# Kernel tuning notes

Hardware: AMD Instinct MI355X
Metric: run time of the kernel (lower is better)

Reference implementation:

```python
import jax, jax.numpy as jnp
import numpy as np

N = 500          # max_neurons, all alive
INPUT_SIZE = 3072
FEAT_DIM = 64
OUT_SIZE = 10
BATCH = 8192
RADIUS = 20.0
VOL = 100.0      # cubic volume (100,100,100)
N_ITER = 3


def setup_inputs() -> dict:
    key = jax.random.key(0)
    k_x, k_pos, k_iw, k_f, k_ow = jax.random.split(key, 5)
    x = jax.random.normal(k_x, (BATCH, INPUT_SIZE), dtype=jnp.float32)
    # seed positions spread across the volume, roughly matching _init_seeds
    positions = jax.random.uniform(k_pos, (N, 3), dtype=jnp.float32) * 80.0 + 10.0
    input_weights = jax.random.normal(k_iw, (N, INPUT_SIZE), dtype=jnp.float32) * 0.02
    features = jax.random.normal(k_f, (N, FEAT_DIM), dtype=jnp.float32) * 0.1
    output_weights = jax.random.normal(k_ow, (N, OUT_SIZE), dtype=jnp.float32) * 0.02
    biases = jnp.zeros((N,), dtype=jnp.float32)
    return {"x": x, "positions": positions, "input_weights": input_weights,
            "features": features, "output_weights": output_weights, "biases": biases}


def reference(x, positions, input_weights, features, output_weights, biases):
    # clamp positions into the volume (per-axis, vol is cubic here)
    pos = jnp.clip(positions, 0.1, VOL - 0.1)  # [N,3]

    # pairwise distances (grad-safe sqrt at the zero diagonal)
    diff = pos[:, None, :] - pos[None, :, :]          # [N,N,3]
    sq = jnp.sum(diff * diff, axis=-1)                # [N,N]
    pos_mask = sq > 0.0
    dist = jnp.where(pos_mask, jnp.sqrt(jnp.where(pos_mask, sq, 1.0)), 0.0)

    conn_mask = (dist < RADIUS) & (dist > 0.0)
    attenuation = jnp.exp(-dist / RADIUS) * conn_mask.astype(dist.dtype)

    # feature similarity (F.normalize clamps the norm from below at eps)
    feat_norm = features / jnp.maximum(
        jnp.linalg.norm(features, axis=1, keepdims=True), 1e-6)
    feat_sim = jnp.clip(feat_norm @ feat_norm.T, -1.0, 1.0)  # [N,N]

    conn_w = attenuation * (0.5 + 0.5 * feat_sim)
    conn_w = conn_w / (jnp.sum(conn_w, axis=1, keepdims=True) + 1e-6)

    # input gating: neurons near x=0 receive input
    x_norm = pos[:, 0] / VOL                          # [N]
    input_weight = jnp.exp(-2.0 * x_norm)
    input_weight = input_weight / (jnp.sum(input_weight) + 1e-6)

    activations = x @ input_weights.T * input_weight + biases  # [B,N]

    # iterative message passing (fixed small iteration count)
    for _ in range(N_ITER):
        msg = activations @ conn_w.T                  # [B,N]
        activations = jnp.minimum(jax.nn.relu(activations + 0.5 * msg), 50.0)

    # output gating: neurons near x=VOL emit output
    output_weight = jnp.exp(2.0 * (x_norm - 1.0))
    output_weight = output_weight / (jnp.sum(output_weight) + 1e-6)

    return activations @ (output_weights * output_weight[:, None])  # [B,OUT]
```

## Files before the change

kernel.cpp:

```cpp
#include <hip/hip_runtime.h>
#include <stdint.h>

#define N_REAL 500
#define NPAD   512
#define K_IN   3072
#define NBATCH 8192
#define NOUT   10
#define RADIUS 20.0f
#define VOLF   100.0f

typedef __attribute__((ext_vector_type(8))) __bf16 bf16x8;
typedef __attribute__((ext_vector_type(4))) float  f32x4;
typedef __attribute__((ext_vector_type(4))) unsigned short us4;

__device__ __forceinline__ unsigned short f2bf(float f) {
    unsigned int u = __float_as_uint(f);
    u += 0x7FFFu + ((u >> 16) & 1u);
    return (unsigned short)(u >> 16);
}
__device__ __forceinline__ float bf2f(unsigned short h) {
    return __uint_as_float(((unsigned int)h) << 16);
}
__device__ __forceinline__ uint2 cvt_pk4(float4 v) {
    uint2 r;
    asm("v_cvt_pk_bf16_f32 %0, %1, %2" : "=v"(r.x) : "v"(v.x), "v"(v.y));
    asm("v_cvt_pk_bf16_f32 %0, %1, %2" : "=v"(r.y) : "v"(v.z), "v"(v.w));
    return r;
}

#define GLOBAL_AS __attribute__((address_space(1)))
#define LDS_AS    __attribute__((address_space(3)))
__device__ __forceinline__ void glds16(const void* g, void* l) {
    __builtin_amdgcn_global_load_lds((const GLOBAL_AS void*)g, (LDS_AS void*)l, 16, 0, 0);
}

__global__ void prep1(const float* __restrict__ positions,
                      const float* __restrict__ features,
                      const float* __restrict__ out_w,
                      const float* __restrict__ biases,
                      float* __restrict__ feat_norm,
                      float* __restrict__ pos_c,
                      float* __restrict__ inw,
                      float* __restrict__ biasp,
                      float* __restrict__ wout)
{
    int n = threadIdx.x;
    float e_in = 0.f, e_out = 0.f;
    float px = 0.f, py = 0.f, pz = 0.f;
    if (n < N_REAL) {
        px = fminf(fmaxf(positions[n*3+0], 0.1f), VOLF - 0.1f);
        py = fminf(fmaxf(positions[n*3+1], 0.1f), VOLF - 0.1f);
        pz = fminf(fmaxf(positions[n*3+2], 0.1f), VOLF - 0.1f);
        float xn = px / VOLF;
        e_in  = expf(-2.f * xn);
        e_out = expf(2.f * (xn - 1.f));
        float ss = 0.f;
        for (int f = 0; f < 64; ++f) { float v = features[n*64+f]; ss += v*v; }
        float nm = fmaxf(sqrtf(ss), 1e-6f);
        for (int f = 0; f < 64; ++f) feat_norm[n*64+f] = features[n*64+f] / nm;
    } else {
        for (int f = 0; f < 64; ++f) feat_norm[n*64+f] = 0.f;
    }
    pos_c[n*4+0] = px; pos_c[n*4+1] = py; pos_c[n*4+2] = pz; pos_c[n*4+3] = 0.f;

    __shared__ float s_in[512], s_out[512];
    s_in[n] = e_in; s_out[n] = e_out;
    __syncthreads();
    for (int s = 256; s > 0; s >>= 1) {
        if (n < s) { s_in[n] += s_in[n+s]; s_out[n] += s_out[n+s]; }
        __syncthreads();
    }
    float sum_in  = s_in[0]  + 1e-6f;
    float sum_out = s_out[0] + 1e-6f;

    inw[n]   = (n < N_REAL) ? (e_in / sum_in) : 0.f;
    biasp[n] = (n < N_REAL) ? biases[n] : 0.f;
    float wo = (n < N_REAL) ? (e_out / sum_out) : 0.f;
    for (int o = 0; o < NOUT; ++o)
        wout[n*NOUT + o] = (n < N_REAL) ? out_w[n*NOUT + o] * wo : 0.f;
}

__global__ void prep2(const float* __restrict__ pos_c,
                      const float* __restrict__ feat_norm,
                      unsigned short* __restrict__ conn_w)
{
    int i = blockIdx.x;
    int t = threadIdx.x;
    __shared__ float fi[64];
    __shared__ float spos[4];
    __shared__ float red[128];
    if (t < 64) fi[t] = feat_norm[i*64 + t];
    if (t < 4)  spos[t] = pos_c[i*4 + t];
    __syncthreads();

    float w[4];
    float part = 0.f;
    for (int jj = 0; jj < 4; ++jj) {
        int j = t + jj*128;
        float val = 0.f;
        if (i < N_REAL && j < N_REAL) {
            float dx = spos[0] - pos_c[j*4+0];
            float dy = spos[1] - pos_c[j*4+1];
            float dz = spos[2] - pos_c[j*4+2];
            float sq = dx*dx + dy*dy + dz*dz;
            if (sq > 0.f) {
                float dist = sqrtf(sq);
                if (dist < RADIUS) {
                    float att = expf(-dist / RADIUS);
                    float sim = 0.f;
                    const float4* fj = (const float4*)(feat_norm + j*64);
                    const float4* fi4 = (const float4*)fi;
                    #pragma unroll
                    for (int f = 0; f < 16; ++f) {
                        float4 a = fi4[f]; float4 b = fj[f];
                        sim += a.x*b.x + a.y*b.y + a.z*b.z + a.w*b.w;
                    }
                    sim = fminf(fmaxf(sim, -1.f), 1.f);
                    val = att * (0.5f + 0.5f*sim);
                }
            }
        }
        w[jj] = val; part += val;
    }
    red[t] = part;
    __syncthreads();
    for (int s = 64; s > 0; s >>= 1) {
        if (t < s) red[t] += red[t+s];
        __syncthreads();
    }
    float inv = 1.f / (red[0] + 1e-6f);
    for (int jj = 0; jj < 4; ++jj)
        conn_w[(long)i*NPAD + t + jj*128] = f2bf(w[jj] * inv);
}

__global__ void cast_pad(const float* __restrict__ src, unsigned short* __restrict__ dst,
                         long total_q, long src_q)
{
    long i = (long)blockIdx.x * blockDim.x + threadIdx.x;
    long stride = (long)gridDim.x * blockDim.x;
    for (; i < total_q; i += stride) {
        us4 o;
        if (i < src_q) {
            float4 v = ((const float4*)src)[i];
            o[0] = f2bf(v.x); o[1] = f2bf(v.y); o[2] = f2bf(v.z); o[3] = f2bf(v.w);
        } else {
            o[0] = 0; o[1] = 0; o[2] = 0; o[3] = 0;
        }
        ((us4*)dst)[i] = o;
    }
}

__device__ __forceinline__ void block_map(int b, int& m0, int& n0) {
    int xcd = b & 7, loc = b >> 3;
    m0 = (xcd*16 + (loc >> 3)) * 64;
    n0 = (loc & 7) * 64;
}

__global__ __launch_bounds__(256)
void gemm1(const float* __restrict__ X,
           const unsigned short* __restrict__ B,
           unsigned short* __restrict__ Cbf,
           const float* __restrict__ inw,
           const float* __restrict__ biasp)
{
    __shared__ unsigned short As[2][64*64];
    __shared__ unsigned short Bs[2][64*64];

    const int tid  = threadIdx.x;
    const int lane = tid & 63;
    const int wave = tid >> 6;
    int m0, n0; block_map(blockIdx.x, m0, n0);
    const int wm = (wave >> 1) * 32;
    const int wn = (wave & 1) * 32;

    f32x4 acc[2][2];
    #pragma unroll
    for (int i = 0; i < 2; ++i)
        #pragma unroll
        for (int j = 0; j < 2; ++j)
            acc[i][j] = (f32x4){0.f,0.f,0.f,0.f};

    const float4* gA[4]; int lAo[4];
    #pragma unroll
    for (int s = 0; s < 4; ++s) {
        int f = tid + s*256;
        int row = f >> 4, c4 = f & 15;
        gA[s] = (const float4*)(X + (long)(m0 + row) * K_IN) + c4;
        lAo[s] = row*128 + ((c4*8) ^ ((row & 7) << 4));
    }
    const char* gB[2]; int lBo[2];
    #pragma unroll
    for (int s = 0; s < 2; ++s) {
        int o = tid*16 + s*4096;
        int row = o >> 7, d = o & 127;
        gB[s] = (const char*)B + (long)(n0 + row) * (K_IN*2) + (d ^ ((row & 7) << 4));
        lBo[s] = o;
    }

    float4 v[4];
    #pragma unroll
    for (int s = 0; s < 4; ++s) { v[s] = gA[s][0]; gA[s] += 16; }
    __builtin_amdgcn_sched_barrier(0);
    glds16(gB[0], (char*)Bs[0] + lBo[0]);
    glds16(gB[1], (char*)Bs[0] + lBo[1]);
    gB[0] += 128; gB[1] += 128;
    #pragma unroll
    for (int s = 0; s < 4; ++s)
        *(uint2*)((char*)As[0] + lAo[s]) = cvt_pk4(v[s]);
    asm volatile("s_waitcnt lgkmcnt(0)" ::: "memory");

    for (int t = 0; t < 48; ++t) {
        const int cur = t & 1;
        const bool more = (t < 47);
        if (more) {
            #pragma unroll
            for (int s = 0; s < 4; ++s) { v[s] = gA[s][0]; gA[s] += 16; }
            __builtin_amdgcn_sched_barrier(0);
            glds16(gB[0], (char*)Bs[cur^1] + lBo[0]);
            glds16(gB[1], (char*)Bs[cur^1] + lBo[1]);
            gB[0] += 128; gB[1] += 128;
            asm volatile("s_waitcnt vmcnt(6)" ::: "memory");
        } else {
            asm volatile("s_waitcnt vmcnt(0)" ::: "memory");
        }
        __builtin_amdgcn_s_barrier();

        #pragma unroll
        for (int kk = 0; kk < 2; ++kk) {
            const int cb = kk*64 + (lane >> 4) * 16;
            bf16x8 afr[2], bfr[2];
            #pragma unroll
            for (int i = 0; i < 2; ++i) {
                int r = wm + i*16 + (lane & 15);
                afr[i] = *(const bf16x8*)((const char*)As[cur] + r*128 + (cb ^ ((r & 7) << 4)));
            }
            #pragma unroll
            for (int j = 0; j < 2; ++j) {
                int r = wn + j*16 + (lane & 15);
                bfr[j] = *(const bf16x8*)((const char*)Bs[cur] + r*128 + (cb ^ ((r & 7) << 4)));
            }
            #pragma unroll
            for (int i = 0; i < 2; ++i)
                #pragma unroll
                for (int j = 0; j < 2; ++j)
                    acc[i][j] = __builtin_amdgcn_mfma_f32_16x16x32_bf16(afr[i], bfr[j], acc[i][j], 0, 0, 0);
        }

        if (more) {
            #pragma unroll
            for (int s = 0; s < 4; ++s)
                *(uint2*)((char*)As[cur^1] + lAo[s]) = cvt_pk4(v[s]);
            asm volatile("s_waitcnt lgkmcnt(0)" ::: "memory");
            __builtin_amdgcn_s_barrier();
        }
    }

    const int mbase = m0 + wm + (lane >> 4) * 4;
    const int nbase = n0 + wn + (lane & 15);
    #pragma unroll
    for (int j = 0; j < 2; ++j) {
        const int n = nbase + j*16;
        const float win = inw[n], bia = biasp[n];
        #pragma unroll
        for (int i = 0; i < 2; ++i)
            #pragma unroll
            for (int r = 0; r < 4; ++r) {
                const long m = mbase + i*16 + r;
                Cbf[m*NPAD + n] = f2bf(acc[i][j][r] * win + bia);
            }
    }
}

__global__ __launch_bounds__(256)
void gemm2(const unsigned short* __restrict__ A,
           const unsigned short* __restrict__ B,
           unsigned short* __restrict__ Cbf,
           const unsigned short* __restrict__ actOld)
{
    __shared__ unsigned short As[2][64*64];
    __shared__ unsigned short Bs[2][64*64];

    const int tid  = threadIdx.x;
    const int lane = tid & 63;
    const int wave = tid >> 6;
    int m0, n0; block_map(blockIdx.x, m0, n0);
    const int wm = (wave >> 1) * 32;
    const int wn = (wave & 1) * 32;

    f32x4 acc[2][2];
    #pragma unroll
    for (int i = 0; i < 2; ++i)
        #pragma unroll
        for (int j = 0; j < 2; ++j)
            acc[i][j] = (f32x4){0.f,0.f,0.f,0.f};

    const char* gA[2]; int lAo[2];
    #pragma unroll
    for (int s = 0; s < 2; ++s) {
        int o = tid*16 + s*4096;
        int row = o >> 7, d = o & 127;
        gA[s] = (const char*)A + (long)(m0 + row) * (NPAD*2) + (d ^ ((row & 7) << 4));
        lAo[s] = o;
    }
    const char* gB[2]; int lBo[2];
    #pragma unroll
    for (int s = 0; s < 2; ++s) {
        int o = tid*16 + s*4096;
        int row = o >> 7, d = o & 127;
        gB[s] = (const char*)B + (long)(n0 + row) * (NPAD*2) + (d ^ ((row & 7) << 4));
        lBo[s] = o;
    }

    #pragma unroll
    for (int s = 0; s < 2; ++s) { glds16(gA[s], (char*)As[0] + lAo[s]); gA[s] += 128; }
    #pragma unroll
    for (int s = 0; s < 2; ++s) { glds16(gB[s], (char*)Bs[0] + lBo[s]); gB[s] += 128; }

    for (int t = 0; t < 8; ++t) {
        const int cur = t & 1;
        const bool more = (t < 7);
        if (more) {
            #pragma unroll
            for (int s = 0; s < 2; ++s) { glds16(gA[s], (char*)As[cur^1] + lAo[s]); gA[s] += 128; }
            #pragma unroll
            for (int s = 0; s < 2; ++s) { glds16(gB[s], (char*)Bs[cur^1] + lBo[s]); gB[s] += 128; }
            asm volatile("s_waitcnt vmcnt(4)" ::: "memory");
        } else {
            asm volatile("s_waitcnt vmcnt(0)" ::: "memory");
        }
        __builtin_amdgcn_s_barrier();

        #pragma unroll
        for (int kk = 0; kk < 2; ++kk) {
            const int cb = kk*64 + (lane >> 4) * 16;
            bf16x8 afr[2], bfr[2];
            #pragma unroll
            for (int i = 0; i < 2; ++i) {
                int r = wm + i*16 + (lane & 15);
                afr[i] = *(const bf16x8*)((const char*)As[cur] + r*128 + (cb ^ ((r & 7) << 4)));
            }
            #pragma unroll
            for (int j = 0; j < 2; ++j) {
                int r = wn + j*16 + (lane & 15);
                bfr[j] = *(const bf16x8*)((const char*)Bs[cur] + r*128 + (cb ^ ((r & 7) << 4)));
            }
            #pragma unroll
            for (int i = 0; i < 2; ++i)
                #pragma unroll
                for (int j = 0; j < 2; ++j)
                    acc[i][j] = __builtin_amdgcn_mfma_f32_16x16x32_bf16(afr[i], bfr[j], acc[i][j], 0, 0, 0);
        }

        if (more)
            __builtin_amdgcn_s_barrier();
    }

    const int mbase = m0 + wm + (lane >> 4) * 4;
    const int nbase = n0 + wn + (lane & 15);
    #pragma unroll
    for (int j = 0; j < 2; ++j) {
        const int n = nbase + j*16;
        #pragma unroll
        for (int i = 0; i < 2; ++i)
            #pragma unroll
            for (int r = 0; r < 4; ++r) {
                const long m = mbase + i*16 + r;
                float old = bf2f(actOld[m*NPAD + n]);
                float vv = fminf(fmaxf(old + 0.5f * acc[i][j][r], 0.f), 50.f);
                Cbf[m*NPAD + n] = f2bf(vv);
            }
    }
}

__global__ __launch_bounds__(256)
void out_gemm(const unsigned short* __restrict__ act,
              const float* __restrict__ wout,
              float* __restrict__ out)
{
    __shared__ float sw[NPAD * NOUT];
    const int tid = threadIdx.x;
    for (int i = tid; i < NPAD*NOUT; i += 256) sw[i] = wout[i];
    __syncthreads();

    const int lane = tid & 63;
    const int wv   = tid >> 6;
    const int row  = blockIdx.x * 4 + wv;

    const unsigned short* ap = act + (long)row * NPAD + lane * 8;
    us4 v0 = *(const us4*)(ap);
    us4 v1 = *(const us4*)(ap + 4);

    float p[NOUT];
    #pragma unroll
    for (int o = 0; o < NOUT; ++o) p[o] = 0.f;

    const int nb = lane * 8;
    #pragma unroll
    for (int e = 0; e < 8; ++e) {
        float a = bf2f(e < 4 ? v0[e] : v1[e-4]);
        const float* wr = &sw[(nb + e) * NOUT];
        #pragma unroll
        for (int o = 0; o < NOUT; ++o) p[o] += a * wr[o];
    }
    #pragma unroll
    for (int o = 0; o < NOUT; ++o) {
        float s = p[o];
        for (int d = 32; d > 0; d >>= 1) s += __shfl_down(s, d);
        if (lane == 0) out[(long)row * NOUT + o] = s;
    }
}

extern "C" void kernel_launch(void* const* d_in, const int* in_sizes, int n_in,
                              void* d_out, int out_size, void* d_ws, size_t ws_size,
                              hipStream_t stream)
{
    const float* x        = (const float*)d_in[0];
    const float* pos      = (const float*)d_in[1];
    const float* in_w     = (const float*)d_in[2];
    const float* feats    = (const float*)d_in[3];
    const float* out_w    = (const float*)d_in[4];
    const float* biases   = (const float*)d_in[5];
    float* out = (float*)d_out;

    char* ws = (char*)d_ws;
    unsigned short* iw_bf  = (unsigned short*)(ws);
    unsigned short* connw  = (unsigned short*)(ws + 3145728);
    unsigned short* act_a  = (unsigned short*)(ws + 3670016);
    unsigned short* act_b  = (unsigned short*)(ws + 12058624);
    float* feat_norm = (float*)(ws + 20447232);
    float* pos_c     = (float*)(ws + 20578304);
    float* inw       = (float*)(ws + 20586496);
    float* biasp     = (float*)(ws + 20588544);
    float* wout      = (float*)(ws + 20590592);

    prep1<<<1, 512, 0, stream>>>(pos, feats, out_w, biases, feat_norm, pos_c, inw, biasp, wout);
    prep2<<<512, 128, 0, stream>>>(pos_c, feat_norm, connw);
    cast_pad<<<512, 256, 0, stream>>>(in_w, iw_bf, 393216L, 384000L);

    gemm1<<<1024, 256, 0, stream>>>(x, iw_bf, act_a, inw, biasp);
    gemm2<<<1024, 256, 0, stream>>>(act_a, connw, act_b, act_a);
    gemm2<<<1024, 256, 0, stream>>>(act_b, connw, act_a, act_b);
    gemm2<<<1024, 256, 0, stream>>>(act_a, connw, act_b, act_a);

    out_gemm<<<NBATCH/4, 256, 0, stream>>>(act_b, wout, out);
}
```

Before: 130.8 us.

## Merge GEMM kernels into templated 64x256-tile kernel with 512 threads

After: 137.3 us. 5.0% more time.

```diff
diff --git a/kernel.cpp b/kernel.cpp
--- a/kernel.cpp
+++ b/kernel.cpp
@@ -152,74 +152,99 @@
 
 __device__ __forceinline__ void block_map(int b, int& m0, int& n0) {
     int xcd = b & 7, loc = b >> 3;
-    m0 = (xcd*16 + (loc >> 3)) * 64;
-    n0 = (loc & 7) * 64;
-}
-
-__global__ __launch_bounds__(256)
-void gemm1(const float* __restrict__ X,
-           const unsigned short* __restrict__ B,
-           unsigned short* __restrict__ Cbf,
-           const float* __restrict__ inw,
-           const float* __restrict__ biasp)
+    m0 = (xcd*16 + (loc >> 1)) * 64;
+    n0 = (loc & 1) * 256;
+}
+
+template<int MODE>
+__global__ __launch_bounds__(512)
+void gemm_main(const float* __restrict__ Xf,
+               const unsigned short* __restrict__ Abf,
+               const unsigned short* __restrict__ B,
+               unsigned short* __restrict__ Cbf,
+               const unsigned short* __restrict__ actOld,
+               const float* __restrict__ inw,
+               const float* __restrict__ biasp,
+               int K)
 {
     __shared__ unsigned short As[2][64*64];
-    __shared__ unsigned short Bs[2][64*64];
+    __shared__ unsigned short Bs[2][256*64];
 
     const int tid  = threadIdx.x;
     const int lane = tid & 63;
     const int wave = tid >> 6;
     int m0, n0; block_map(blockIdx.x, m0, n0);
-    const int wm = (wave >> 1) * 32;
-    const int wn = (wave & 1) * 32;
-
-    f32x4 acc[2][2];
+    const int wm = (wave >> 2) * 32;
+    const int wn = (wave & 3) * 64;
+
+    f32x4 acc[2][4];
     #pragma unroll
     for (int i = 0; i < 2; ++i)
         #pragma unroll
-        for (int j = 0; j < 2; ++j)
+        for (int j = 0; j < 4; ++j)
             acc[i][j] = (f32x4){0.f,0.f,0.f,0.f};
 
-    const float4* gA[4]; int lAo[4];
+    const char* gB[4]; int lBo[4];
     #pragma unroll
     for (int s = 0; s < 4; ++s) {
-        int f = tid + s*256;
-        int row = f >> 4, c4 = f & 15;
-        gA[s] = (const float4*)(X + (long)(m0 + row) * K_IN) + c4;
-        lAo[s] = row*128 + ((c4*8) ^ ((row & 7) << 4));
-    }
-    const char* gB[2]; int lBo[2];
-    #pragma unroll
-    for (int s = 0; s < 2; ++s) {
-        int o = tid*16 + s*4096;
+        int o = tid*16 + s*8192;
         int row = o >> 7, d = o & 127;
-        gB[s] = (const char*)B + (long)(n0 + row) * (K_IN*2) + (d ^ ((row & 7) << 4));
+        gB[s] = (const char*)B + (long)(n0 + row) * (K*2) + (d ^ ((row & 7) << 4));
         lBo[s] = o;
     }
-
-    float4 v[4];
-    #pragma unroll
-    for (int s = 0; s < 4; ++s) { v[s] = gA[s][0]; gA[s] += 16; }
-    __builtin_amdgcn_sched_barrier(0);
-    glds16(gB[0], (char*)Bs[0] + lBo[0]);
-    glds16(gB[1], (char*)Bs[0] + lBo[1]);
-    gB[0] += 128; gB[1] += 128;
-    #pragma unroll
-    for (int s = 0; s < 4; ++s)
-        *(uint2*)((char*)As[0] + lAo[s]) = cvt_pk4(v[s]);
-    asm volatile("s_waitcnt lgkmcnt(0)" ::: "memory");
-
-    for (int t = 0; t < 48; ++t) {
+    const float4* gA[2]; int lAo[2];
+    const char* gA1 = nullptr; int lAo1 = 0;
+    if (MODE == 0) {
+        #pragma unroll
+        for (int s = 0; s < 2; ++s) {
+            int f = tid + s*512;
+            int row = f >> 4, c4 = f & 15;
+            gA[s] = (const float4*)(Xf + (long)(m0 + row) * K) + c4;
+            lAo[s] = row*128 + ((c4*8) ^ ((row & 7) << 4));
+        }
+    } else {
+        int o = tid*16;
+        int row = o >> 7, d = o & 127;
+        gA1 = (const char*)Abf + (long)(m0 + row) * (K*2) + (d ^ ((row & 7) << 4));
+        lAo1 = o;
+    }
+
+    const int NT = K >> 6;
+
+    float4 v[2];
+    if (MODE == 0) {
+        #pragma unroll
+        for (int s = 0; s < 2; ++s) { v[s] = gA[s][0]; gA[s] += 16; }
+        __builtin_amdgcn_sched_barrier(0);
+    } else {
+        glds16(gA1, (char*)As[0] + lAo1); gA1 += 128;
+    }
+    #pragma unroll
+    for (int s = 0; s < 4; ++s) { glds16(gB[s], (char*)Bs[0] + lBo[s]); gB[s] += 128; }
+    if (MODE == 0) {
+        #pragma unroll
+        for (int s = 0; s < 2; ++s)
+            *(uint2*)((char*)As[0] + lAo[s]) = cvt_pk4(v[s]);
+        asm volatile("s_waitcnt lgkmcnt(0)" ::: "memory");
+    }
+
+    for (int t = 0; t < NT; ++t) {
         const int cur = t & 1;
-        const bool more = (t < 47);
+        const bool more = (t < NT-1);
         if (more) {
-            #pragma unroll
-            for (int s = 0; s < 4; ++s) { v[s] = gA[s][0]; gA[s] += 16; }
-            __builtin_amdgcn_sched_barrier(0);
-            glds16(gB[0], (char*)Bs[cur^1] + lBo[0]);
-            glds16(gB[1], (char*)Bs[cur^1] + lBo[1]);
-            gB[0] += 128; gB[1] += 128;
-            asm volatile("s_waitcnt vmcnt(6)" ::: "memory");
+            if (MODE == 0) {
+                #pragma unroll
+                for (int s = 0; s < 2; ++s) { v[s] = gA[s][0]; gA[s] += 16; }
+                __builtin_amdgcn_sched_barrier(0);
+                #pragma unroll
+                for (int s = 0; s < 4; ++s) { glds16(gB[s], (char*)Bs[cur^1] + lBo[s]); gB[s] += 128; }
+                asm volatile("s_waitcnt vmcnt(6)" ::: "memory");
+            } else {
+                glds16(gA1, (char*)As[cur^1] + lAo1); gA1 += 128;
+                #pragma unroll
+                for (int s = 0; s < 4; ++s) { glds16(gB[s], (char*)Bs[cur^1] + lBo[s]); gB[s] += 128; }
+                asm volatile("s_waitcnt vmcnt(5)" ::: "memory");
+            }
         } else {
             asm volatile("s_waitcnt vmcnt(0)" ::: "memory");
         }
@@ -228,29 +253,31 @@
         #pragma unroll
         for (int kk = 0; kk < 2; ++kk) {
             const int cb = kk*64 + (lane >> 4) * 16;
-            bf16x8 afr[2], bfr[2];
+            bf16x8 afr[2], bfr[4];
             #pragma unroll
             for (int i = 0; i < 2; ++i) {
                 int r = wm + i*16 + (lane & 15);
                 afr[i] = *(const bf16x8*)((const char*)As[cur] + r*128 + (cb ^ ((r & 7) << 4)));
             }
             #pragma unroll
-            for (int j = 0; j < 2; ++j) {
+            for (int j = 0; j < 4; ++j) {
                 int r = wn + j*16 + (lane & 15);
                 bfr[j] = *(const bf16x8*)((const char*)Bs[cur] + r*128 + (cb ^ ((r & 7) << 4)));
             }
             #pragma unroll
             for (int i = 0; i < 2; ++i)
                 #pragma unroll
-                for (int j = 0; j < 2; ++j)
+                for (int j = 0; j < 4; ++j)
                     acc[i][j] = __builtin_amdgcn_mfma_f32_16x16x32_bf16(afr[i], bfr[j], acc[i][j], 0, 0, 0);
         }
 
         if (more) {
-            #pragma unroll
-            for (int s = 0; s < 4; ++s)
-                *(uint2*)((char*)As[cur^1] + lAo[s]) = cvt_pk4(v[s]);
-            asm volatile("s_waitcnt lgkmcnt(0)" ::: "memory");
+            if (MODE == 0) {
+                #pragma unroll
+                for (int s = 0; s < 2; ++s)
+                    *(uint2*)((char*)As[cur^1] + lAo[s]) = cvt_pk4(v[s]);
+                asm volatile("s_waitcnt lgkmcnt(0)" ::: "memory");
+            }
             __builtin_amdgcn_s_barrier();
         }
     }
@@ -258,115 +285,22 @@
     const int mbase = m0 + wm + (lane >> 4) * 4;
     const int nbase = n0 + wn + (lane & 15);
     #pragma unroll
-    for (int j = 0; j < 2; ++j) {
+    for (int j = 0; j < 4; ++j) {
         const int n = nbase + j*16;
-        const float win = inw[n], bia = biasp[n];
+        float win = 0.f, bia = 0.f;
+        if (MODE == 0) { win = inw[n]; bia = biasp[n]; }
         #pragma unroll
         for (int i = 0; i < 2; ++i)
             #pragma unroll
             for (int r = 0; r < 4; ++r) {
                 const long m = mbase + i*16 + r;
-                Cbf[m*NPAD + n] = f2bf(acc[i][j][r] * win + bia);
-            }
-    }
-}
-
-__global__ __launch_bounds__(256)
-void gemm2(const unsigned short* __restrict__ A,
-           const unsigned short* __restrict__ B,
-           unsigned short* __restrict__ Cbf,
-           const unsigned short* __restrict__ actOld)
-{
-    __shared__ unsigned short As[2][64*64];
-    __shared__ unsigned short Bs[2][64*64];
-
-    const int tid  = threadIdx.x;
-    const int lane = tid & 63;
-    const int wave = tid >> 6;
-    int m0, n0; block_map(blockIdx.x, m0, n0);
-    const int wm = (wave >> 1) * 32;
-    const int wn = (wave & 1) * 32;
-
-    f32x4 acc[2][2];
-    #pragma unroll
-    for (int i = 0; i < 2; ++i)
-        #pragma unroll
-        for (int j = 0; j < 2; ++j)
-            acc[i][j] = (f32x4){0.f,0.f,0.f,0.f};
-
-    const char* gA[2]; int lAo[2];
-    #pragma unroll
-    for (int s = 0; s < 2; ++s) {
-        int o = tid*16 + s*4096;
-        int row = o >> 7, d = o & 127;
-        gA[s] = (const char*)A + (long)(m0 + row) * (NPAD*2) + (d ^ ((row & 7) << 4));
-        lAo[s] = o;
-    }
-    const char* gB[2]; int lBo[2];
-    #pragma unroll
-    for (int s = 0; s < 2; ++s) {
-        int o = tid*16 + s*4096;
-        int row = o >> 7, d = o & 127;
-        gB[s] = (const char*)B + (long)(n0 + row) * (NPAD*2) + (d ^ ((row & 7) << 4));
-        lBo[s] = o;
-    }
-
-    #pragma unroll
-    for (int s = 0; s < 2; ++s) { glds16(gA[s], (char*)As[0] + lAo[s]); gA[s] += 128; }
-    #pragma unroll
-    for (int s = 0; s < 2; ++s) { glds16(gB[s], (char*)Bs[0] + lBo[s]); gB[s] += 128; }
-
-    for (int t = 0; t < 8; ++t) {
-        const int cur = t & 1;
-        const bool more = (t < 7);
-        if (more) {
-            #pragma unroll
-            for (int s = 0; s < 2; ++s) { glds16(gA[s], (char*)As[cur^1] + lAo[s]); gA[s] += 128; }
-            #pragma unroll
-            for (int s = 0; s < 2; ++s) { glds16(gB[s], (char*)Bs[cur^1] + lBo[s]); gB[s] += 128; }
-            asm volatile("s_waitcnt vmcnt(4)" ::: "memory");
-        } else {
-            asm volatile("s_waitcnt vmcnt(0)" ::: "memory");
-        }
-        __builtin_amdgcn_s_barrier();
-
-        #pragma unroll
-        for (int kk = 0; kk < 2; ++kk) {
-            const int cb = kk*64 + (lane >> 4) * 16;
-            bf16x8 afr[2], bfr[2];
-            #pragma unroll
-            for (int i = 0; i < 2; ++i) {
-                int r = wm + i*16 + (lane & 15);
-                afr[i] = *(const bf16x8*)((const char*)As[cur] + r*128 + (cb ^ ((r & 7) << 4)));
-            }
-            #pragma unroll
-            for (int j = 0; j < 2; ++j) {
-                int r = wn + j*16 + (lane & 15);
-                bfr[j] = *(const bf16x8*)((const char*)Bs[cur] + r*128 + (cb ^ ((r & 7) << 4)));
-            }
-            #pragma unroll
-            for (int i = 0; i < 2; ++i)
-                #pragma unroll
-                for (int j = 0; j < 2; ++j)
-                    acc[i][j] = __builtin_amdgcn_mfma_f32_16x16x32_bf16(afr[i], bfr[j], acc[i][j], 0, 0, 0);
-        }
-
-        if (more)
-            __builtin_amdgcn_s_barrier();
-    }
-
-    const int mbase = m0 + wm + (lane >> 4) * 4;
-    const int nbase = n0 + wn + (lane & 15);
-    #pragma unroll
-    for (int j = 0; j < 2; ++j) {
-        const int n = nbase + j*16;
-        #pragma unroll
-        for (int i = 0; i < 2; ++i)
-            #pragma unroll
-            for (int r = 0; r < 4; ++r) {
-                const long m = mbase + i*16 + r;
-                float old = bf2f(actOld[m*NPAD + n]);
-                float vv = fminf(fmaxf(old + 0.5f * acc[i][j][r], 0.f), 50.f);
+                float vv;
+                if (MODE == 0) {
+                    vv = acc[i][j][r] * win + bia;
+                } else {
+                    float old = bf2f(actOld[m*NPAD + n]);
+                    vv = fminf(fmaxf(old + 0.5f * acc[i][j][r], 0.f), 50.f);
+                }
                 Cbf[m*NPAD + n] = f2bf(vv);
             }
     }
@@ -437,10 +371,10 @@
     prep2<<<512, 128, 0, stream>>>(pos_c, feat_norm, connw);
     cast_pad<<<512, 256, 0, stream>>>(in_w, iw_bf, 393216L, 384000L);
 
-    gemm1<<<1024, 256, 0, stream>>>(x, iw_bf, act_a, inw, biasp);
-    gemm2<<<1024, 256, 0, stream>>>(act_a, connw, act_b, act_a);
-    gemm2<<<1024, 256, 0, stream>>>(act_b, connw, act_a, act_b);
-    gemm2<<<1024, 256, 0, stream>>>(act_a, connw, act_b, act_a);
+    gemm_main<0><<<256, 512, 0, stream>>>(x, nullptr, iw_bf, act_a, nullptr, inw, biasp, K_IN);
+    gemm_main<1><<<256, 512, 0, stream>>>(nullptr, act_a, connw, act_b, act_a, nullptr, nullptr, NPAD);
+    gemm_main<1><<<256, 512, 0, stream>>>(nullptr, act_b, connw, act_a, act_b, nullptr, nullptr, NPAD);
+    gemm_main<1><<<256, 512, 0, stream>>>(nullptr, act_a, connw, act_b, act_a, nullptr, nullptr, NPAD);
 
     out_gemm<<<NBATCH/4, 256, 0, stream>>>(act_b, wout, out);
 }
```
